# Optimization experiments

Measured on AMD Instinct MI355X. Metric: run time of the kernel, lower is better.

The kernel has to match this reference:

```python
import jax, jax.numpy as jnp
import numpy as np

N_HEADS = 16
WINDOW = 256  # window_size; keep keys with |i-j| <= WINDOW//2


def setup_inputs() -> dict:
    key = jax.random.key(0)
    ks = jax.random.split(key, 6)
    B, S, D = 2, 2048, 1024
    x = jax.random.normal(ks[0], (B, S, D), dtype=jnp.float32)
    # torch nn.Linear weights are [out_features, in_features]
    scale = 1.0 / np.sqrt(D)
    Wq = jax.random.normal(ks[1], (D, D), dtype=jnp.float32) * scale
    Wk = jax.random.normal(ks[2], (D, D), dtype=jnp.float32) * scale
    Wv = jax.random.normal(ks[3], (D, D), dtype=jnp.float32) * scale
    Wo = jax.random.normal(ks[4], (D, D), dtype=jnp.float32) * scale
    # standard ALiBi slopes: 2^(-8*(h+1)/H)
    slopes = jnp.asarray(2.0 ** (-8.0 * (np.arange(1, N_HEADS + 1) / N_HEADS)), dtype=jnp.float32)
    return {"x": x, "Wq": Wq, "Wk": Wk, "Wv": Wv, "Wo": Wo, "slopes": slopes}


def reference(x, Wq, Wk, Wv, Wo, slopes):
    B, S, D = x.shape
    H = N_HEADS
    dk = D // H
    # projections (torch Linear: y = x @ W.T)
    q = jnp.einsum('bsd,od->bso', x, Wq).reshape(B, S, H, dk)
    k = jnp.einsum('bsd,od->bso', x, Wk).reshape(B, S, H, dk)
    v = jnp.einsum('bsd,od->bso', x, Wv).reshape(B, S, H, dk)
    # full score matrix [B,H,S,S]
    scores = jnp.einsum('bqhd,bkhd->bhqk', q, k) / jnp.sqrt(jnp.asarray(dk, x.dtype))
    pos = jnp.arange(S)
    rel = (pos[:, None] - pos[None, :]).astype(x.dtype)          # [S,S] q_pos - k_pos
    scores = scores + slopes[None, :, None, None] * rel[None, None]
    window_mask = jnp.abs(pos[:, None] - pos[None, :]) <= (WINDOW // 2)  # [S,S]
    scores = jnp.where(window_mask[None, None], scores, -jnp.inf)
    attn = jax.nn.softmax(scores, axis=-1)
    out = jnp.einsum('bhqk,bkhd->bqhd', attn, v).reshape(B, S, D)
    return jnp.einsum('bsd,od->bso', out, Wo)
```

## Files before the change

### kernel.cpp

```cpp
#include <hip/hip_runtime.h>
#include <hip/hip_bf16.h>

#define S_LEN   2048
#define D_MODEL 1024
#define NH      16
#define DK      64
#define BATCH   2
#define M_ROWS  (BATCH * S_LEN)
#define LDP     72
#define LDV     66
#define LDW     132

typedef __attribute__((ext_vector_type(8))) short bf16x8;
typedef __attribute__((ext_vector_type(4))) float f32x4;
typedef __attribute__((ext_vector_type(16))) float f32x16;
typedef __attribute__((ext_vector_type(8))) unsigned short us8;
typedef __attribute__((ext_vector_type(4))) unsigned short us4;

static __device__ __forceinline__ unsigned short f2bf(float f) {
    unsigned u = __builtin_bit_cast(unsigned, f);
    u += 0x7fffu + ((u >> 16) & 1u);
    return (unsigned short)(u >> 16);
}

__global__ __launch_bounds__(256) void cvt_all(const float* __restrict__ x,
                                               const float* __restrict__ wq,
                                               const float* __restrict__ wk,
                                               const float* __restrict__ wv,
                                               const float* __restrict__ wo,
                                               unsigned short* __restrict__ dst) {
    const int b = blockIdx.x;
    if (b < 2048) {
        const size_t o8 = (size_t)b * 256 + threadIdx.x;
        const float4* s = (const float4*)x + o8 * 2;
        float4 a = s[0], bb = s[1];
        us8 o;
        o[0] = f2bf(a.x);  o[1] = f2bf(a.y);  o[2] = f2bf(a.z);  o[3] = f2bf(a.w);
        o[4] = f2bf(bb.x); o[5] = f2bf(bb.y); o[6] = f2bf(bb.z); o[7] = f2bf(bb.w);
        *((us8*)dst + o8) = o;
    } else {
        const int wi = (b - 2048) >> 9;
        const float* src = (wi == 0) ? wq : (wi == 1) ? wk : (wi == 2) ? wv : wo;
        const size_t local = (size_t)((b - 2048) & 511) * 256 + threadIdx.x;
        const float4* s = (const float4*)src + local * 2;
        float4 a = s[0], bb = s[1];
        us8 o;
        o[0] = f2bf(a.x);  o[1] = f2bf(a.y);  o[2] = f2bf(a.z);  o[3] = f2bf(a.w);
        o[4] = f2bf(bb.x); o[5] = f2bf(bb.y); o[6] = f2bf(bb.z); o[7] = f2bf(bb.w);
        *((us8*)dst + 524288 + (size_t)wi * 131072 + local) = o;
    }
}

template <int STORE_BF16, int BN>
__global__ __launch_bounds__(256) void mfma_gemm_bt(const unsigned short* __restrict__ A,
                                                    const unsigned short* __restrict__ W,
                                                    void* __restrict__ Cv, int N) {
    constexpr int K = 1024, BM = 128, BK = 64;
    constexpr int MI = (BN == 128) ? 2 : 1;
    constexpr int SMEM = (STORE_BF16 && BN == 128) ? (128 * LDW)
                                                   : (BM * BK + BN * BK);
    __shared__ unsigned short smem[SMEM];
    unsigned short* As = smem;
    unsigned short* Bs = smem + BM * BK;

    const int tid  = threadIdx.x;
    const int w    = tid >> 6;
    const int lane = tid & 63;
    const int m0 = blockIdx.y * BM;
    const int n0 = blockIdx.x * BN;
    const int wr = (BN == 128) ? (w >> 1) * 64 : w * 32;
    const int wc = (BN == 128) ? (w & 1) * 64 : 0;

    const int srow   = lane >> 3;
    const int schunk = ((lane & 7) ^ (lane >> 3)) * 8;
    const int l31   = lane & 31;
    const int khalf = lane >> 5;
    const int sw    = lane & 7;
    int roff[4];
#pragma unroll
    for (int s = 0; s < 4; ++s)
        roff[s] = ((2 * s + khalf) ^ sw) * 8;

    f32x16 acc[MI][2] = {};

    for (int k0 = 0; k0 < K; k0 += BK) {
        __syncthreads();
#pragma unroll
        for (int t = 0; t < 4; ++t) {
            const int rbase = w * 32 + t * 8;
            const unsigned short* ga = A + (size_t)(m0 + rbase + srow) * K + k0 + schunk;
            __builtin_amdgcn_global_load_lds(
                (const __attribute__((address_space(1))) void*)ga,
                (__attribute__((address_space(3))) void*)(As + rbase * BK), 16, 0, 0);
        }
#pragma unroll
        for (int t = 0; t < BN / 32; ++t) {
            const int rbase = w * (BN / 4) + t * 8;
            const unsigned short* gb = W + (size_t)(n0 + rbase + srow) * K + k0 + schunk;
            __builtin_amdgcn_global_load_lds(
                (const __attribute__((address_space(1))) void*)gb,
                (__attribute__((address_space(3))) void*)(Bs + rbase * BK), 16, 0, 0);
        }
        __syncthreads();

#pragma unroll
        for (int s = 0; s < 4; ++s) {
            bf16x8 af[MI], bfr[2];
#pragma unroll
            for (int i = 0; i < MI; ++i)
                af[i] = *(const bf16x8*)(As + (wr + i * 32 + l31) * BK + roff[s]);
#pragma unroll
            for (int j = 0; j < 2; ++j)
                bfr[j] = *(const bf16x8*)(Bs + (wc + j * 32 + l31) * BK + roff[s]);
#pragma unroll
            for (int i = 0; i < MI; ++i)
#pragma unroll
                for (int j = 0; j < 2; ++j)
                    acc[i][j] = __builtin_amdgcn_mfma_f32_32x32x16_bf16(af[i], bfr[j], acc[i][j], 0, 0, 0);
        }
    }

    if constexpr (STORE_BF16 && BN == 128) {
        __syncthreads();
#pragma unroll
        for (int i = 0; i < 2; ++i)
#pragma unroll
            for (int j = 0; j < 2; ++j)
#pragma unroll
                for (int r = 0; r < 16; ++r) {
                    const int row_l = wr + i * 32 + (r & 3) + 8 * (r >> 2) + 4 * khalf;
                    const int col_l = wc + j * 32 + l31;
                    smem[row_l * LDW + col_l] = f2bf(acc[i][j][r]);
                }
        __syncthreads();
#pragma unroll
        for (int e = 0; e < 8; ++e) {
            const int idx = e * 256 + tid;
            const int row = idx >> 4;
            const int cc  = (idx & 15) * 8;
            us4 lo = *(const us4*)(smem + row * LDW + cc);
            us4 hi = *(const us4*)(smem + row * LDW + cc + 4);
            us8 v;
            v[0] = lo[0]; v[1] = lo[1]; v[2] = lo[2]; v[3] = lo[3];
            v[4] = hi[0]; v[5] = hi[1]; v[6] = hi[2]; v[7] = hi[3];
            *(us8*)((unsigned short*)Cv + (size_t)(m0 + row) * N + n0 + cc) = v;
        }
    } else {
#pragma unroll
        for (int i = 0; i < MI; ++i)
#pragma unroll
            for (int j = 0; j < 2; ++j)
#pragma unroll
                for (int r = 0; r < 16; ++r) {
                    const int gm = m0 + wr + i * 32 + (r & 3) + 8 * (r >> 2) + 4 * khalf;
                    const int gn = n0 + wc + j * 32 + l31;
                    if (STORE_BF16)
                        ((unsigned short*)Cv)[(size_t)gm * N + gn] = f2bf(acc[i][j][r]);
                    else
                        ((float*)Cv)[(size_t)gm * N + gn] = acc[i][j][r];
                }
    }
}

__global__ __launch_bounds__(256) void attn_mfma(const unsigned short* __restrict__ qkvb,
                                                 const float* __restrict__ slopes,
                                                 unsigned short* __restrict__ aoutb) {
    __shared__ unsigned short QPs[64 * LDP];
    __shared__ unsigned short Ks[2 * 64 * 64];
    __shared__ unsigned short Vt[64 * LDV];

    const int tid  = threadIdx.x;
    const int w    = tid >> 6;
    const int lane = tid & 63;
    const int q0 = blockIdx.x * 64;
    const int h  = blockIdx.y;
    const int b  = blockIdx.z;
    const float slope = slopes[h];
    const size_t rowbase = (size_t)b * S_LEN * 3072;

#pragma unroll
    for (int e = 0; e < 2; ++e) {
        int idx = e * 256 + tid;
        int r = idx >> 3, cc = (idx & 7) * 8;
        us8 v = *(const us8*)(qkvb + rowbase + (size_t)(q0 + r) * 3072 + h * DK + cc);
        *(us8*)(QPs + r * LDP + cc) = v;
    }

    const int col = lane & 15;
    const int rq  = (lane >> 4) * 4;
    const int wq  = w * 16;
    const int fo  = (lane >> 4) * 8;

    const int srowK   = lane >> 3;
    const int schunkK = ((lane & 7) ^ srowK) * 8;
    const int kc0 = (((lane >> 4) + 0) ^ (lane & 7)) * 8;
    const int kc1 = (((lane >> 4) + 4) ^ (lane & 7)) * 8;

    const unsigned short* kbase  = qkvb + rowbase + 1024 + h * DK;
    const unsigned short* vbase0 = qkvb + rowbase + 2048 + h * DK;

    const int rp  = tid >> 3;
    const int ccv = (tid & 7) * 8;

    float qa[4];
#pragma unroll
    for (int r = 0; r < 4; ++r) {
        const int qpos = q0 + wq + rq + r;
        qa[r] = slope * (float)(qpos > 128 ? qpos - 128 : 0) - 12.0f;
    }

    f32x4 o_acc[4] = {};
    float l_part[4] = {0.f, 0.f, 0.f, 0.f};

    {
        const int k0 = q0 - 128;
#pragma unroll
        for (int t = 0; t < 2; ++t) {
            const int rbase = w * 16 + t * 8;
            const unsigned short* gk = kbase + (long long)(k0 + rbase + srowK) * 3072 + schunkK;
            __builtin_amdgcn_global_load_lds(
                (const __attribute__((address_space(1))) void*)gk,
                (__attribute__((address_space(3))) void*)(Ks + rbase * 64), 16, 0, 0);
        }
        const long long kp0 = (long long)(k0 + rp * 2);
        us8 v0 = *(const us8*)(vbase0 + ccv + kp0 * 3072);
        us8 v1 = *(const us8*)(vbase0 + ccv + (kp0 + 1) * 3072);
#pragma unroll
        for (int t = 0; t < 8; ++t) {
            unsigned pk = (unsigned)(unsigned short)v0[t] | ((unsigned)(unsigned short)v1[t] << 16);
            *(unsigned*)(Vt + (ccv + t) * LDV + rp * 2) = pk;
        }
    }
    __syncthreads();

    const bf16x8 aq0 = *(const bf16x8*)(QPs + (wq + col) * LDP + fo);
    const bf16x8 aq1 = *(const bf16x8*)(QPs + (wq + col) * LDP + fo + 32);

    int cur = 0;
    for (int c = 0; c < 5; ++c) {
        const int k0 = q0 - 128 + c * 64;
        const unsigned short* KsC = Ks + cur * 4096;
        const bool have_next = (c < 4);

        us8 nv0, nv1;
        if (have_next) {
            const int kn0 = k0 + 64;
            unsigned short* KsN = (unsigned short*)Ks + (cur ^ 1) * 4096;
#pragma unroll
            for (int t = 0; t < 2; ++t) {
                const int rbase = w * 16 + t * 8;
                const unsigned short* gk = kbase + (long long)(kn0 + rbase + srowK) * 3072 + schunkK;
                __builtin_amdgcn_global_load_lds(
                    (const __attribute__((address_space(1))) void*)gk,
                    (__attribute__((address_space(3))) void*)(KsN + rbase * 64), 16, 0, 0);
            }
            const long long kp0 = (long long)(kn0 + rp * 2);
            nv0 = *(const us8*)(vbase0 + ccv + kp0 * 3072);
            nv1 = *(const us8*)(vbase0 + ccv + (kp0 + 1) * 3072);
        }

        f32x4 sacc[4] = {};
        __builtin_amdgcn_s_setprio(1);
#pragma unroll
        for (int j = 0; j < 4; ++j) {
            const int tt  = wq - 64 * c - 16 * j;
            const int klo = k0 + 16 * j;
            const bool any_v = (tt <= 0) && (tt >= -256) && (klo < S_LEN) && (klo + 15 >= 0);
            if (any_v) {
                bf16x8 bk0 = *(const bf16x8*)(KsC + (j * 16 + col) * 64 + kc0);
                bf16x8 bk1 = *(const bf16x8*)(KsC + (j * 16 + col) * 64 + kc1);
                sacc[j] = __builtin_amdgcn_mfma_f32_16x16x32_bf16(aq0, bk0, sacc[j], 0, 0, 0);
                sacc[j] = __builtin_amdgcn_mfma_f32_16x16x32_bf16(aq1, bk1, sacc[j], 0, 0, 0);
            }
        }
        __builtin_amdgcn_s_setprio(0);

#pragma unroll
        for (int j = 0; j < 4; ++j) {
            const int tt  = wq - 64 * c - 16 * j;
            const int klo = k0 + 16 * j;
            const bool any_v = (tt <= 0) && (tt >= -256) && (klo < S_LEN) && (klo + 15 >= 0);
            unsigned short* ps = QPs + (wq + rq) * LDP + j * 16 + col;
            if (!any_v) {
#pragma unroll
                for (int r = 0; r < 4; ++r) ps[r * LDP] = 0;
            } else {
                const float kb = slope * (float)(klo + col);
                const bool all_v = (tt <= -16) && (tt >= -240) && (klo >= 0) && (klo + 15 < S_LEN);
                if (all_v) {
#pragma unroll
                    for (int r = 0; r < 4; ++r) {
                        float p = __expf(fmaf(sacc[j][r], 0.125f, qa[r] - kb));
                        l_part[r] += p;
                        ps[r * LDP] = f2bf(p);
                    }
                } else {
                    const int kpos = klo + col;
                    const bool kin = (unsigned)kpos < (unsigned)S_LEN;
#pragma unroll
                    for (int r = 0; r < 4; ++r) {
                        const int rel = (q0 + wq + rq + r) - kpos;
                        const bool ok = kin && (rel <= 128) && (rel >= -128);
                        float p = 0.f;
                        if (ok) p = __expf(fmaf(sacc[j][r], 0.125f, qa[r] - kb));
                        l_part[r] += p;
                        ps[r * LDP] = f2bf(p);
                    }
                }
            }
        }

        {
            bf16x8 ap0 = *(const bf16x8*)(QPs + (wq + col) * LDP + fo);
            bf16x8 ap1 = *(const bf16x8*)(QPs + (wq + col) * LDP + fo + 32);
            __builtin_amdgcn_s_setprio(1);
#pragma unroll
            for (int j = 0; j < 4; ++j) {
                bf16x8 bv0 = *(const bf16x8*)(Vt + (j * 16 + col) * LDV + fo);
                bf16x8 bv1 = *(const bf16x8*)(Vt + (j * 16 + col) * LDV + fo + 32);
                o_acc[j] = __builtin_amdgcn_mfma_f32_16x16x32_bf16(ap0, bv0, o_acc[j], 0, 0, 0);
                o_acc[j] = __builtin_amdgcn_mfma_f32_16x16x32_bf16(ap1, bv1, o_acc[j], 0, 0, 0);
            }
            __builtin_amdgcn_s_setprio(0);
        }

        if (have_next) {
            __syncthreads();
#pragma unroll
            for (int t = 0; t < 8; ++t) {
                unsigned pk = (unsigned)(unsigned short)nv0[t] | ((unsigned)(unsigned short)nv1[t] << 16);
                *(unsigned*)(Vt + (ccv + t) * LDV + rp * 2) = pk;
            }
            __syncthreads();
        }
        cur ^= 1;
    }

    float inv[4];
#pragma unroll
    for (int r = 0; r < 4; ++r) {
        float l = l_part[r];
#pragma unroll
        for (int off = 1; off < 16; off <<= 1) l += __shfl_xor(l, off, 64);
        inv[r] = 1.f / l;
    }

#pragma unroll
    for (int j = 0; j < 4; ++j)
#pragma unroll
        for (int r = 0; r < 4; ++r) {
            const int qpos = q0 + wq + rq + r;
            aoutb[((size_t)b * S_LEN + qpos) * D_MODEL + h * DK + j * 16 + col] =
                f2bf(o_acc[j][r] * inv[r]);
        }
}

extern "C" void kernel_launch(void* const* d_in, const int* in_sizes, int n_in,
                              void* d_out, int out_size, void* d_ws, size_t ws_size,
                              hipStream_t stream) {
    const float* x      = (const float*)d_in[0];
    const float* Wq     = (const float*)d_in[1];
    const float* Wk     = (const float*)d_in[2];
    const float* Wv     = (const float*)d_in[3];
    const float* Wo     = (const float*)d_in[4];
    const float* slopes = (const float*)d_in[5];
    float* out = (float*)d_out;

    unsigned short* xb    = (unsigned short*)d_ws;
    unsigned short* wb    = xb    + (size_t)M_ROWS * D_MODEL;
    unsigned short* wob   = wb    + (size_t)3072 * D_MODEL;
    unsigned short* qkvb  = wob   + (size_t)1024 * D_MODEL;
    unsigned short* aoutb = qkvb  + (size_t)M_ROWS * 3072;

    dim3 blk(256);
    cvt_all<<<4096, blk, 0, stream>>>(x, Wq, Wk, Wv, Wo, xb);
    mfma_gemm_bt<1, 128><<<dim3(3072 / 128, M_ROWS / 128), blk, 0, stream>>>(xb, wb, qkvb, 3072);
    attn_mfma<<<dim3(S_LEN / 64, NH, BATCH), blk, 0, stream>>>(qkvb, slopes, aoutb);
    mfma_gemm_bt<0, 64><<<dim3(1024 / 64, M_ROWS / 128), blk, 0, stream>>>(aoutb, wob, out, 1024);
}
```

Baseline: 154.1 us.

## Add 256x256-tile QKV GEMM with direct global-to-LDS double buffering

Replaces the 128x128-tile QKV projection GEMM with a new 512-thread kernel that computes 256x256 output tiles, giving more operand reuse per loaded byte. Operands are streamed with global_load_lds into XOR-swizzled, double-buffered shared memory, and the next K tile's loads are interleaved with MFMA issue. The kernel also raises wave priority around the MFMA bursts and stages the bf16 results through LDS for coalesced stores. The cost is a 128 KB LDS footprint and only 192 blocks for the GPU's CUs, so occupancy and load balance may suffer.

```diff
diff --git a/kernel.cpp b/kernel.cpp
--- a/kernel.cpp
+++ b/kernel.cpp
@@ -51,6 +51,102 @@
     }
 }
 
+__global__ __launch_bounds__(512, 2) void gemm_qkv_256(const unsigned short* __restrict__ A,
+                                                       const unsigned short* __restrict__ W,
+                                                       unsigned short* __restrict__ C) {
+    __shared__ unsigned short smem[65536];
+    const int tid  = threadIdx.x;
+    const int w    = tid >> 6;
+    const int lane = tid & 63;
+    const int wm = w >> 2;
+    const int wn = w & 3;
+    const int m0 = blockIdx.y * 256;
+    const int n0 = blockIdx.x * 256;
+
+    const int srow   = lane >> 3;
+    const int schunk = ((lane & 7) ^ srow) * 8;
+    const int w16    = w * 16;
+    const int l15    = lane & 15;
+    int roff[2];
+    roff[0] = (((lane >> 4) + 0) ^ (lane & 7)) * 8;
+    roff[1] = (((lane >> 4) + 4) ^ (lane & 7)) * 8;
+
+    f32x4 acc[8][4] = {};
+
+    auto stage = [&](const unsigned short* gsrc, int gbase, int kt_, int half,
+                     int dbuf, int isB) {
+        unsigned short* dst = smem + isB * 32768 + (dbuf * 2 + half) * 8192 + w16 * 64;
+        const unsigned short* g = gsrc + (size_t)(gbase + half * 128 + w16 + srow) * 1024
+                                  + kt_ * 64 + schunk;
+        __builtin_amdgcn_global_load_lds(
+            (const __attribute__((address_space(1))) void*)g,
+            (__attribute__((address_space(3))) void*)dst, 16, 0, 0);
+        __builtin_amdgcn_global_load_lds(
+            (const __attribute__((address_space(1))) void*)(g + 8 * 1024),
+            (__attribute__((address_space(3))) void*)(dst + 8 * 64), 16, 0, 0);
+    };
+
+    stage(A, m0, 0, 0, 0, 0); stage(A, m0, 0, 1, 0, 0);
+    stage(W, n0, 0, 0, 0, 1); stage(W, n0, 0, 1, 0, 1);
+    asm volatile("s_waitcnt vmcnt(0)\ns_barrier" ::: "memory");
+
+    for (int kt = 0; kt < 16; ++kt) {
+        const int buf = kt & 1;
+        const unsigned short* Abase = smem + (buf * 2 + wm) * 8192;
+        const unsigned short* Bbase = smem + 32768 + (buf * 2 + (wn >> 1)) * 8192;
+        const int brow = (wn & 1) * 64;
+#pragma unroll
+        for (int q = 0; q < 4; ++q) {
+            const int rh = q >> 1, ks = q & 1;
+            bf16x8 af[4], bfr[4];
+#pragma unroll
+            for (int i = 0; i < 4; ++i)
+                af[i] = *(const bf16x8*)(Abase + (rh * 64 + i * 16 + l15) * 64 + roff[ks]);
+#pragma unroll
+            for (int j = 0; j < 4; ++j)
+                bfr[j] = *(const bf16x8*)(Bbase + (brow + j * 16 + l15) * 64 + roff[ks]);
+            if (kt < 15) {
+                if (q == 0) { stage(A, m0, kt + 1, 0, buf ^ 1, 0);
+                              stage(A, m0, kt + 1, 1, buf ^ 1, 0); }
+                else if (q == 1) { stage(W, n0, kt + 1, 0, buf ^ 1, 1);
+                                   stage(W, n0, kt + 1, 1, buf ^ 1, 1); }
+            }
+            if (q == 3) asm volatile("s_waitcnt vmcnt(0)" ::: "memory");
+            asm volatile("s_barrier" ::: "memory");
+            __builtin_amdgcn_s_setprio(1);
+#pragma unroll
+            for (int i = 0; i < 4; ++i)
+#pragma unroll
+                for (int j = 0; j < 4; ++j)
+                    acc[rh * 4 + i][j] = __builtin_amdgcn_mfma_f32_16x16x32_bf16(
+                        af[i], bfr[j], acc[rh * 4 + i][j], 0, 0, 0);
+            __builtin_amdgcn_s_setprio(0);
+            asm volatile("s_barrier" ::: "memory");
+        }
+    }
+
+    __syncthreads();
+#pragma unroll
+    for (int a = 0; a < 8; ++a)
+#pragma unroll
+        for (int j = 0; j < 4; ++j)
+#pragma unroll
+            for (int r = 0; r < 4; ++r) {
+                const int lr = wm * 128 + (a >> 2) * 64 + (a & 3) * 16 + (lane >> 4) * 4 + r;
+                const int lc = wn * 64 + j * 16 + l15;
+                smem[lr * 256 + lc] = f2bf(acc[a][j][r]);
+            }
+    __syncthreads();
+#pragma unroll
+    for (int e = 0; e < 16; ++e) {
+        const int idx = e * 512 + tid;
+        const int lr = idx >> 5;
+        const int sl = idx & 31;
+        us8 v = *(const us8*)(smem + lr * 256 + sl * 8);
+        *(us8*)(C + (size_t)(m0 + lr) * 3072 + n0 + sl * 8) = v;
+    }
+}
+
 template <int STORE_BF16, int BN>
 __global__ __launch_bounds__(256) void mfma_gemm_bt(const unsigned short* __restrict__ A,
                                                     const unsigned short* __restrict__ W,
@@ -374,7 +470,7 @@
 
     dim3 blk(256);
     cvt_all<<<4096, blk, 0, stream>>>(x, Wq, Wk, Wv, Wo, xb);
-    mfma_gemm_bt<1, 128><<<dim3(3072 / 128, M_ROWS / 128), blk, 0, stream>>>(xb, wb, qkvb, 3072);
+    gemm_qkv_256<<<dim3(3072 / 256, M_ROWS / 256), dim3(512), 0, stream>>>(xb, wb, qkvb);
     attn_mfma<<<dim3(S_LEN / 64, NH, BATCH), blk, 0, stream>>>(qkvb, slopes, aoutb);
     mfma_gemm_bt<0, 64><<<dim3(1024 / 64, M_ROWS / 128), blk, 0, stream>>>(aoutb, wob, out, 1024);
 }
```

After: 158.7 us. +3.0%, slower.
